# Kernel tuning notes

Measured on AMD Instinct MI355X. Metric: run time of the kernel, lower is better.

## Reference

```python
import jax, jax.numpy as jnp
import numpy as np
from jax import lax

L = 12  # db6 filter length
REC_LO = np.array([0.11154074335008017, 0.4946238903983854, 0.7511339080215775,
                   0.3152503517092432, -0.22626469396516913, -0.12976686756709563,
                   0.09750160558707936, 0.02752286553001629, -0.031582039318031156,
                   0.0005538422009938016, 0.004777257511010651, -0.00107730108499558])
DEC_LO = REC_LO[::-1]
_sgn = (-1.0) ** np.arange(L)
DEC_HI = -_sgn * REC_LO            # pywt dec_hi
REC_HI = _sgn * DEC_LO             # pywt rec_hi
# XLA conv = cross-correlation; pytorch_wavelets correlates with reversed dec filters
K_ANA = np.ascontiguousarray(np.stack([DEC_LO[::-1], DEC_HI[::-1]])[:, None, :])  # (2,1,12)
# conv_transpose(stride2, pad L-2) == dilate-by-2, pad 1, correlate with flipped rec filters
K_SYN = np.ascontiguousarray(np.stack([REC_LO[::-1], REC_HI[::-1]])[None, :, :])  # (1,2,12)
J = 8


def _afb(x):
    # one analysis level, symmetric mode (pytorch_wavelets afb1d)
    B, C, N = x.shape
    out = (N + L - 1) // 2
    p = 2 * (out - 1) - N + L
    xp = jnp.pad(x, ((0, 0), (0, 0), (p // 2, p - p // 2)), mode='symmetric')
    y = lax.conv_general_dilated(xp.reshape(B * C, 1, -1), jnp.asarray(K_ANA, x.dtype),
                                 (2,), 'VALID', dimension_numbers=('NCH', 'OIH', 'NCH'))
    y = y.reshape(B, C, 2, out)
    return y[:, :, 0], y[:, :, 1]


def _sfb(lo, hi):
    # one synthesis level (pytorch_wavelets sfb1d); crop lo to hi length first
    lo = lo[..., :hi.shape[-1]]
    B, C, N = lo.shape
    z = jnp.stack([lo, hi], 2).reshape(B * C, 2, N)
    y = lax.conv_general_dilated(z, jnp.asarray(K_SYN, lo.dtype), (1,), [(1, 1)],
                                 lhs_dilation=(2,), dimension_numbers=('NCH', 'OIH', 'NCH'))
    return y.reshape(B, C, -1)  # length 2N - L + 2


def _wave_conv(x, w1, w2):
    lo, highs = x, []
    for _ in range(J):
        lo, hi = _afb(lo)
        highs.append(hi)
    lo = jnp.einsum('bix,iox->box', lo, w1)
    highs[-1] = jnp.einsum('bix,iox->box', highs[-1], w2)
    for hi in highs[::-1]:
        lo = _sfb(lo, hi)
    return lo


def _branch(xg, fc0_w, fc0_b, ww1, ww2, cw, cb, fc1_w, fc1_b, fc2_w, fc2_b):
    v = jnp.transpose(xg @ fc0_w + fc0_b, (0, 2, 1))  # (B,C,S)
    for i in range(4):
        a = _wave_conv(v, ww1[i], ww2[i])
        b = jnp.einsum('bcs,oc->bos', v, cw[i]) + cb[i][None, :, None]
        v = a + b
        if i < 3:
            v = jax.nn.gelu(v, approximate=False)
    v = jnp.transpose(v, (0, 2, 1))
    v = jax.nn.gelu(v @ fc1_w + fc1_b, approximate=False)
    return v @ fc2_w + fc2_b


def setup_inputs() -> dict:
    key = jax.random.key(0)
    ks = iter(jax.random.split(key, 32))
    B, S, W, LV = 64, 1024, 64, 8
    d = {"x": jax.random.normal(next(ks), (B, S, 1), jnp.float32)}
    def params(pref):
        sc = 1.0 / (W * W)
        d[pref + "fc0_w"] = jax.random.normal(next(ks), (2, W), jnp.float32) * 0.5
        d[pref + "fc0_b"] = jax.random.normal(next(ks), (W,), jnp.float32) * 0.1
        d[pref + "wave_w1"] = sc * jax.random.uniform(next(ks), (4, W, W, LV + 6), jnp.float32)
        d[pref + "wave_w2"] = sc * jax.random.uniform(next(ks), (4, W, W, LV + 6), jnp.float32)
        d[pref + "cw"] = jax.random.normal(next(ks), (4, W, W), jnp.float32) * (1.0 / np.sqrt(W))
        d[pref + "cb"] = jax.random.normal(next(ks), (4, W), jnp.float32) * 0.05
        d[pref + "fc1_w"] = jax.random.normal(next(ks), (W, 128), jnp.float32) * (1.0 / np.sqrt(W))
        d[pref + "fc1_b"] = jax.random.normal(next(ks), (128,), jnp.float32) * 0.05
        d[pref + "fc2_w"] = jax.random.normal(next(ks), (128, 1), jnp.float32) * (1.0 / np.sqrt(128))
        d[pref + "fc2_b"] = jax.random.normal(next(ks), (1,), jnp.float32) * 0.05
    params("")
    params("nt_")
    return d


def reference(x, fc0_w, fc0_b, wave_w1, wave_w2, cw, cb, fc1_w, fc1_b, fc2_w, fc2_b,
              nt_fc0_w, nt_fc0_b, nt_wave_w1, nt_wave_w2, nt_cw, nt_cb,
              nt_fc1_w, nt_fc1_b, nt_fc2_w, nt_fc2_b):
    B, S, _ = x.shape
    grid = jnp.broadcast_to(jnp.linspace(0.0, 1.0, S, dtype=x.dtype)[None, :, None], (B, S, 1))
    xg = jnp.concatenate([x, grid], -1)
    y = _branch(xg, fc0_w, fc0_b, wave_w1, wave_w2, cw, cb, fc1_w, fc1_b, fc2_w, fc2_b)
    y_nt = _branch(xg, nt_fc0_w, nt_fc0_b, nt_wave_w1, nt_wave_w2, nt_cw, nt_cb,
                   nt_fc1_w, nt_fc1_b, nt_fc2_w, nt_fc2_b)
    return y + y_nt
```

## Files before the change

### kernel.cpp

```cpp
#include <hip/hip_runtime.h>
#include <hip/hip_bf16.h>
#include <math.h>


#define BDIM 64
#define SLEN 1024
#define WCH  64
#define BC   (BDIM*WCH)
#define NT   16

typedef short s16x8 __attribute__((ext_vector_type(8)));
typedef float f32x4 __attribute__((ext_vector_type(4)));
typedef unsigned short u16x4 __attribute__((ext_vector_type(4)));

constexpr float RLv[12] = {
    0.11154074335008017f, 0.4946238903983854f, 0.7511339080215775f,
    0.3152503517092432f, -0.22626469396516913f, -0.12976686756709563f,
    0.09750160558707936f, 0.02752286553001629f, -0.031582039318031156f,
    0.0005538422009938016f, 0.004777257511010651f, -0.00107730108499558f };
constexpr float AHv[12] = {
     RLv[11], -RLv[10],  RLv[9], -RLv[8],  RLv[7], -RLv[6],
     RLv[5],  -RLv[4],   RLv[3], -RLv[2],  RLv[1], -RLv[0] };
constexpr float SLv[12] = {
     RLv[11], RLv[10], RLv[9], RLv[8], RLv[7], RLv[6],
     RLv[5],  RLv[4],  RLv[3], RLv[2], RLv[1], RLv[0] };
constexpr float SHv[12] = {
    -RLv[0],  RLv[1], -RLv[2],  RLv[3], -RLv[4],  RLv[5],
    -RLv[6],  RLv[7], -RLv[8],  RLv[9], -RLv[10], RLv[11] };

__device__ __forceinline__ float gelu_f(float x) {
    float z = 0.7978845608f * (x + 0.044715f * x * x * x);
    return x / (1.0f + __expf(-2.0f * z));
}
__device__ __forceinline__ unsigned short f2bf(float f) {
    __hip_bfloat16 h = __float2bfloat16(f);
    union { __hip_bfloat16 h; unsigned short u; } cv; cv.h = h; return cv.u;
}
__device__ __forceinline__ float bf2f(unsigned short u) {
    union { unsigned short u; __hip_bfloat16 h; } cv; cv.u = u;
    return __bfloat162float(cv.h);
}
__device__ __forceinline__ void unpack_frag(const unsigned int* p8,
                                            s16x8* ah, s16x8* al) {
    uint4 a = *(const uint4*)p8;
    uint4 b = *(const uint4*)(p8 + 4);
    union { s16x8 v; unsigned int d[4]; } H, L;
    H.d[0] = __builtin_amdgcn_perm(a.y, a.x, 0x05040100u);
    H.d[1] = __builtin_amdgcn_perm(a.w, a.z, 0x05040100u);
    H.d[2] = __builtin_amdgcn_perm(b.y, b.x, 0x05040100u);
    H.d[3] = __builtin_amdgcn_perm(b.w, b.z, 0x05040100u);
    L.d[0] = __builtin_amdgcn_perm(a.y, a.x, 0x07060302u);
    L.d[1] = __builtin_amdgcn_perm(a.w, a.z, 0x07060302u);
    L.d[2] = __builtin_amdgcn_perm(b.y, b.x, 0x07060302u);
    L.d[3] = __builtin_amdgcn_perm(b.w, b.z, 0x07060302u);
    *ah = H.v; *al = L.v;
}

__device__ __forceinline__ int swz(int c, int s) {
    return c * 64 + ((((s >> 3) ^ (c & 7)) << 3) | (s & 7));
}
__device__ __forceinline__ int swz2(int s, int c) {
    return s * 64 + ((((c >> 3) ^ (s & 7)) << 3) | (c & 7));
}

__device__ __forceinline__ void proj2(
    const unsigned short* Phi, const unsigned short* Plo,
    const unsigned short* __restrict__ Ahi, const unsigned short* __restrict__ Alo,
    float* __restrict__ Ppart, int bb, int tile, int s0, int t)
{
    const int lane = t & 63;
    const int w    = t >> 6;
    const int qr   = lane >> 4;
    const int ln   = lane & 15;

    f32x4 pacc[2][2];
#pragma unroll
    for (int mt = 0; mt < 2; ++mt)
#pragma unroll
        for (int ni = 0; ni < 2; ++ni) pacc[mt][ni] = (f32x4){0.f,0.f,0.f,0.f};

#pragma unroll
    for (int kk = 0; kk < 2; ++kk) {
        const int bk = kk * 4 + qr;
        s16x8 pah[2], pal[2];
#pragma unroll
        for (int mt = 0; mt < 2; ++mt) {
            const int arow = (mt * 16 + ln) * SLEN + s0 + kk * 32 + qr * 8;
            pah[mt] = *(const s16x8*)&Ahi[arow];
            pal[mt] = *(const s16x8*)&Alo[arow];
        }
#pragma unroll
        for (int ni = 0; ni < 2; ++ni) {
            const int c = w * 32 + ni * 16 + ln;
            const int boff = c * 64 + ((bk ^ (c & 7)) << 3);
            s16x8 bh = *(const s16x8*)&Phi[boff];
            s16x8 bl = *(const s16x8*)&Plo[boff];
#pragma unroll
            for (int mt = 0; mt < 2; ++mt) {
                pacc[mt][ni] = __builtin_amdgcn_mfma_f32_16x16x32_bf16(pah[mt], bh, pacc[mt][ni], 0, 0, 0);
                pacc[mt][ni] = __builtin_amdgcn_mfma_f32_16x16x32_bf16(pal[mt], bh, pacc[mt][ni], 0, 0, 0);
                pacc[mt][ni] = __builtin_amdgcn_mfma_f32_16x16x32_bf16(pah[mt], bl, pacc[mt][ni], 0, 0, 0);
            }
        }
    }
#pragma unroll
    for (int mt = 0; mt < 2; ++mt)
#pragma unroll
        for (int ni = 0; ni < 2; ++ni) {
            const int c = w * 32 + ni * 16 + ln;
#pragma unroll
            for (int r = 0; r < 4; ++r) {
                const int xr = mt * 16 + qr * 4 + r;
                if (xr < 28)
                    Ppart[((size_t)(bb * NT + tile) * 28 + xr) * 64 + c] = pacc[mt][ni][r];
            }
        }
}

__global__ __launch_bounds__(256) void setup_kernel(
    const float* __restrict__ x,
    unsigned short* __restrict__ Ahi, unsigned short* __restrict__ Alo,
    unsigned short* __restrict__ MThi, unsigned short* __restrict__ MTlo,
    float* __restrict__ axbuf,
    const float* __restrict__ fc1w_0, const float* __restrict__ fc1w_1,
    const float* __restrict__ cw_0, const float* __restrict__ cw_1,
    unsigned short* __restrict__ w1hi, unsigned short* __restrict__ w1lo,
    unsigned short* __restrict__ cwPhi, unsigned short* __restrict__ cwPlo,
    unsigned short* __restrict__ Dhi,  unsigned short* __restrict__ Dlo)
{
    __shared__ float Af[1024];
    __shared__ float Bff[520];
    __shared__ float hib[14];
    const int t = threadIdx.x;

    if (blockIdx.x < 1024 || (blockIdx.x >= 1052 && blockIdx.x < 1118)) {
        const bool isA = (blockIdx.x < 1024);
        const int s0 = blockIdx.x;
        const int di = blockIdx.x - 1052;
        for (int i = t; i < SLEN; i += 256) {
            float v;
            if (isA)           v = (i == s0) ? 1.0f : 0.0f;
            else if (di < 64)  v = x[di * SLEN + i];
            else if (di == 64) v = (float)i * (1.0f / 1023.0f);
            else               v = 1.0f;
            Af[i] = v;
        }
        __syncthreads();

        const int NIN[8]  = {1024, 517, 264, 137, 74, 42, 26, 18};
        const int NOUT[8] = { 517, 264, 137,  74, 42, 26, 18, 14};
#pragma unroll
        for (int lev = 0; lev < 8; ++lev) {
            float* in  = (lev & 1) ? Bff : Af;
            float* out = (lev & 1) ? Af : Bff;
            const int nin = NIN[lev], nout = NOUT[lev];
            for (int m = t; m < nout; m += 256) {
                float alo = 0.f, ahi = 0.f;
#pragma unroll
                for (int tt = 0; tt < 12; ++tt) {
                    int jj = 2 * m + tt - 10;
                    if (jj < 0)         jj = -1 - jj;
                    else if (jj >= nin) jj = 2 * nin - 1 - jj;
                    float xv = in[jj];
                    alo += xv * RLv[tt];
                    if (lev == 7) ahi += xv * AHv[tt];
                }
                out[m] = alo;
                if (lev == 7) {
                    if (isA) {
                        unsigned short h1 = f2bf(alo);
                        Ahi[m * SLEN + s0] = h1;
                        Alo[m * SLEN + s0] = f2bf(alo - bf2f(h1));
                        unsigned short h2 = f2bf(ahi);
                        Ahi[(14 + m) * SLEN + s0] = h2;
                        Alo[(14 + m) * SLEN + s0] = f2bf(ahi - bf2f(h2));
                    } else {
                        axbuf[di * 28 + m]      = alo;
                        axbuf[di * 28 + 14 + m] = ahi;
                    }
                }
            }
            __syncthreads();
        }
        if (isA && t < 4) {
            Ahi[(28 + t) * SLEN + s0] = 0; Alo[(28 + t) * SLEN + s0] = 0;
            MThi[s0 * 32 + 28 + t] = 0;    MTlo[s0 * 32 + 28 + t] = 0;
        }
        return;
    }

    if (blockIdx.x >= 1118) {
        const int gid = (blockIdx.x - 1118) * 256 + t;
        for (int idx = gid; idx < 16384; idx += 2048) {
            int br = idx >> 13, r = idx & 8191;
            int h = r >> 6, c = r & 63;
            float f = (br ? fc1w_1 : fc1w_0)[c * 128 + h];
            unsigned short hh = f2bf(f);
            w1hi[idx] = hh;
            w1lo[idx] = f2bf(f - bf2f(hh));
        }
        for (int idx = gid; idx < 32768; idx += 2048) {
            int L = idx >> 13, br = (idx >> 12) & 1, e = idx & 4095;
            int k = e >> 6, o = e & 63;
            float val = (br ? cw_1 : cw_0)[(size_t)L * 4096 + o * 64 + k]
                      + ((k == o) ? 1.0f : 0.0f);
            unsigned short h = f2bf(val);
            const int off = (L * 2 + br) * 4096 + o * 64 + k;
            cwPhi[off] = h;
            cwPlo[off] = f2bf(val - bf2f(h));
        }
        for (int idx = gid; idx < 32768; idx += 2048) {
            int bb = idx >> 8, o = (idx >> 2) & 63, j = idx & 3;
            Dhi[bb * 2048 + o * 32 + 28 + j] = 0;
            Dlo[bb * 2048 + o * 32 + 28 + j] = 0;
        }
        return;
    }

    const int u = blockIdx.x - 1024;
    if (t < 14) {
        Af[t]  = (u < 14 && t == u) ? 1.0f : 0.0f;
        hib[t] = (u >= 14 && t == (u - 14)) ? 1.0f : 0.0f;
    }
    __syncthreads();

    const int NH[8] = {14, 18, 26, 42, 74, 137, 264, 517};
    const int NO[8] = {18, 26, 42, 74, 138, 264, 518, 1024};

#pragma unroll
    for (int s = 0; s < 8; ++s) {
        const float* lo = (s & 1) ? Bff : Af;
        float* out      = (s & 1) ? Af : Bff;
        const int N = NH[s], nout = NO[s];
        for (int m = t; m < nout; m += 256) {
            float acc = 0.f;
#pragma unroll
            for (int tt = 0; tt < 12; ++tt) {
                int uu = m + tt - 1;
                if ((uu & 1) == 0) {
                    int q = uu >> 1;
                    if (q < N) {
                        acc += lo[q] * SLv[tt];
                        if (s == 0) acc += hib[q] * SHv[tt];
                    }
                }
            }
            out[m] = acc;
        }
        __syncthreads();
    }
    for (int m = t; m < SLEN; m += 256) {
        float f = Af[m];
        unsigned short h = f2bf(f);
        MThi[m * 32 + u] = h;
        MTlo[m * 32 + u] = f2bf(f - bf2f(h));
    }
}

__global__ __launch_bounds__(256) void mix0_kernel(
    const float* __restrict__ axbuf,
    const float* __restrict__ fc0w_0, const float* __restrict__ fc0b_0,
    const float* __restrict__ fc0w_1, const float* __restrict__ fc0b_1,
    const float* __restrict__ w1_0, const float* __restrict__ w2_0,
    const float* __restrict__ w1_1, const float* __restrict__ w2_1,
    unsigned short* __restrict__ Dhi, unsigned short* __restrict__ Dlo)
{
    const int t = threadIdx.x;
    const int br  = blockIdx.x / 224;
    const int sub = blockIdx.x % 224;

    __shared__ float Ws[64][65];
    __shared__ float LO[8][64];
    const int o = t & 63;
    const int w = t >> 6;
    const int x  = sub >> 3;
    const int b0 = (sub & 7) << 3;

    const float* wbase = (x < 14) ? (br ? w1_1 : w1_0) : (br ? w2_1 : w2_0);
    const int xi = (x < 14) ? x : (x - 14);
    for (int idx = t; idx < 4096; idx += 256)
        Ws[idx >> 6][idx & 63] = wbase[(size_t)idx * 14 + xi];

    const float* fc0w = br ? fc0w_1 : fc0w_0;
    const float* fc0b = br ? fc0b_1 : fc0b_0;
    const float agv = axbuf[64 * 28 + x];
    const float a1v = axbuf[65 * 28 + x];
    const float w0o = fc0w[o];
    const float wgo = fc0w[WCH + o];
    const float b0o = fc0b[o];

#pragma unroll
    for (int j = 0; j < 2; ++j) {
        int bi = w + 4 * j;
        int b  = b0 + bi;
        float axv = axbuf[b * 28 + x];
        LO[bi][o] = axv * w0o + agv * wgo + a1v * b0o;
    }
    __syncthreads();

#pragma unroll
    for (int j = 0; j < 2; ++j) {
        int bi = w + 4 * j;
        int bb = br * 64 + b0 + bi;
        float acc = 0.f;
        for (int i = 0; i < 64; ++i)
            acc += LO[bi][i] * Ws[i][o];
        acc -= LO[bi][o];
        unsigned short h = f2bf(acc);
        Dhi[bb * 2048 + o * 32 + x] = h;
        Dlo[bb * 2048 + o * 32 + x] = f2bf(acc - bf2f(h));
    }
}

__global__ __launch_bounds__(256) void mix_kernel(
    const float* __restrict__ Ppart,
    const float* __restrict__ w1_0, const float* __restrict__ w2_0,
    const float* __restrict__ w1_1, const float* __restrict__ w2_1,
    unsigned short* __restrict__ Dhi, unsigned short* __restrict__ Dlo)
{
    const int t = threadIdx.x;
    const int br  = blockIdx.x / 224;
    const int sub = blockIdx.x % 224;

    __shared__ float Ws[64][65];
    __shared__ float LO[8][64];
    const int o = t & 63;
    const int w = t >> 6;
    const int x  = sub >> 3;
    const int b0 = (sub & 7) << 3;

    const float* wbase = (x < 14) ? (br ? w1_1 : w1_0) : (br ? w2_1 : w2_0);
    const int xi = (x < 14) ? x : (x - 14);
    for (int idx = t; idx < 4096; idx += 256)
        Ws[idx >> 6][idx & 63] = wbase[(size_t)idx * 14 + xi];

#pragma unroll
    for (int j = 0; j < 2; ++j) {
        int bi = w + 4 * j;
        int bb = br * 64 + b0 + bi;
        float s = 0.f;
        for (int tile = 0; tile < NT; ++tile)
            s += Ppart[((size_t)(bb * NT + tile) * 28 + x) * 64 + o];
        LO[bi][o] = s;
    }
    __syncthreads();

#pragma unroll
    for (int j = 0; j < 2; ++j) {
        int bi = w + 4 * j;
        int bb = br * 64 + b0 + bi;
        float acc = 0.f;
        for (int i = 0; i < 64; ++i)
            acc += LO[bi][i] * Ws[i][o];
        acc -= LO[bi][o];
        unsigned short h = f2bf(acc);
        Dhi[bb * 2048 + o * 32 + x] = h;
        Dlo[bb * 2048 + o * 32 + x] = f2bf(acc - bf2f(h));
    }
}

__global__ __launch_bounds__(128, 3) void layer_kernel(
    const unsigned int* __restrict__ vin0, const unsigned int* __restrict__ vin1,
    unsigned int* __restrict__ vout0, unsigned int* __restrict__ vout1,
    const unsigned short* __restrict__ MThi, const unsigned short* __restrict__ MTlo,
    const unsigned short* __restrict__ Ahi,  const unsigned short* __restrict__ Alo,
    const unsigned short* __restrict__ cwPhi, const unsigned short* __restrict__ cwPlo,
    const unsigned short* __restrict__ Dhi,   const unsigned short* __restrict__ Dlo,
    const float* __restrict__ cb_0, const float* __restrict__ cb_1,
    const float* __restrict__ fc0w_0, const float* __restrict__ fc0b_0,
    const float* __restrict__ fc0w_1, const float* __restrict__ fc0b_1,
    const float* __restrict__ xin,
    float* __restrict__ Ppart, int Lidx)
{
    __shared__ unsigned short Phi[4096];
    __shared__ unsigned short Plo[4096];

    const int t = threadIdx.x;
    const int bid = blockIdx.x;
    const int br  = bid >> 10;
    const int rem = bid & 1023;
    const int b    = rem >> 4;
    const int tile = rem & 15;
    const int s0   = tile << 6;
    const size_t bS = (size_t)b * SLEN;
    const unsigned int* vin = br ? vin1 : vin0;
    unsigned int* vout      = br ? vout1 : vout0;
    const float* cb = br ? cb_1 : cb_0;
    const float* f0w = br ? fc0w_1 : fc0w_0;
    const float* f0b = br ? fc0b_1 : fc0b_0;
    const int bb = br * 64 + b;
    const int cwbase = (Lidx * 2 + br) * 4096;

    const int lane = t & 63;
    const int w    = t >> 6;
    const int qr   = lane >> 4;
    const int ln   = lane & 15;

    s16x8 Bh[2][2], Bl[2][2];
#pragma unroll
    for (int kk = 0; kk < 2; ++kk)
#pragma unroll
        for (int ni = 0; ni < 2; ++ni) {
            const int o = w * 32 + ni * 16 + ln;
            const int boff = cwbase + o * 64 + kk * 32 + qr * 8;
            Bh[kk][ni] = *(const s16x8*)&cwPhi[boff];
            Bl[kk][ni] = *(const s16x8*)&cwPlo[boff];
        }
    s16x8 Dhf[2], Dlf[2];
#pragma unroll
    for (int ni = 0; ni < 2; ++ni) {
        const int o = w * 32 + ni * 16 + ln;
        const int boff = bb * 2048 + o * 32 + qr * 8;
        Dhf[ni] = *(const s16x8*)&Dhi[boff];
        Dlf[ni] = *(const s16x8*)&Dlo[boff];
    }
    float cbv[2];
#pragma unroll
    for (int ni = 0; ni < 2; ++ni) cbv[ni] = cb[w * 32 + ni * 16 + ln];

#pragma unroll
    for (int mi = 0; mi < 4; ++mi) {
        const int srow = mi * 16 + ln;
        f32x4 acc[2];
        acc[0] = (f32x4){0.f,0.f,0.f,0.f};
        acc[1] = (f32x4){0.f,0.f,0.f,0.f};

#pragma unroll
        for (int kk = 0; kk < 2; ++kk) {
            s16x8 ah, al;
            if (Lidx == 0) {
                const int s = s0 + srow;
                const float xv = xin[bS + s];
                const float gv = (float)s * (1.0f / 1023.0f);
#pragma unroll
                for (int j = 0; j < 8; ++j) {
                    const int c = kk * 32 + qr * 8 + j;
                    float val = xv * f0w[c] + gv * f0w[WCH + c] + f0b[c];
                    unsigned short h = f2bf(val);
                    ah[j] = (short)h;
                    al[j] = (short)f2bf(val - bf2f(h));
                }
            } else {
                const size_t aoff = (bS + s0 + srow) * 64 + kk * 32 + qr * 8;
                unpack_frag(&vin[aoff], &ah, &al);
            }
#pragma unroll
            for (int ni = 0; ni < 2; ++ni) {
                acc[ni] = __builtin_amdgcn_mfma_f32_16x16x32_bf16(ah, Bh[kk][ni], acc[ni], 0, 0, 0);
                acc[ni] = __builtin_amdgcn_mfma_f32_16x16x32_bf16(al, Bh[kk][ni], acc[ni], 0, 0, 0);
                acc[ni] = __builtin_amdgcn_mfma_f32_16x16x32_bf16(ah, Bl[kk][ni], acc[ni], 0, 0, 0);
            }
        }
        {
            const size_t aoff = (size_t)(s0 + srow) * 32 + qr * 8;
            s16x8 ah = *(const s16x8*)&MThi[aoff];
            s16x8 al = *(const s16x8*)&MTlo[aoff];
#pragma unroll
            for (int ni = 0; ni < 2; ++ni) {
                acc[ni] = __builtin_amdgcn_mfma_f32_16x16x32_bf16(ah, Dhf[ni], acc[ni], 0, 0, 0);
                acc[ni] = __builtin_amdgcn_mfma_f32_16x16x32_bf16(al, Dhf[ni], acc[ni], 0, 0, 0);
                acc[ni] = __builtin_amdgcn_mfma_f32_16x16x32_bf16(ah, Dlf[ni], acc[ni], 0, 0, 0);
            }
        }
#pragma unroll
        for (int ni = 0; ni < 2; ++ni) {
            const int o = w * 32 + ni * 16 + ln;
            u16x4 hv, lv;
#pragma unroll
            for (int r = 0; r < 4; ++r) {
                const int sl64 = mi * 16 + qr * 4 + r;
                float val = gelu_f(acc[ni][r] + cbv[ni]);
                unsigned short h = f2bf(val);
                unsigned short l = f2bf(val - bf2f(h));
                vout[(bS + s0 + sl64) * 64 + o] =
                    (unsigned int)h | ((unsigned int)l << 16);
                hv[r] = h;
                lv[r] = l;
            }
            const int a = swz(o, mi * 16 + qr * 4);
            *(u16x4*)&Phi[a] = hv;
            *(u16x4*)&Plo[a] = lv;
        }
    }

    proj2(Phi, Plo, Ahi, Alo, Ppart, bb, tile, s0, t);
}

__global__ __launch_bounds__(256, 2) void head_kernel(
    const unsigned int* __restrict__ vin0, const unsigned int* __restrict__ vin1,
    const unsigned short* __restrict__ MThi, const unsigned short* __restrict__ MTlo,
    const unsigned short* __restrict__ cwPhi, const unsigned short* __restrict__ cwPlo,
    const unsigned short* __restrict__ Dhi,   const unsigned short* __restrict__ Dlo,
    const float* __restrict__ cb_0, const float* __restrict__ cb_1,
    const unsigned short* __restrict__ w1hi, const unsigned short* __restrict__ w1lo,
    const float* __restrict__ fc1b_0, const float* __restrict__ fc2w_0,
    const float* __restrict__ fc2b_0,
    const float* __restrict__ fc1b_1, const float* __restrict__ fc2w_1,
    const float* __restrict__ fc2b_1,
    float* __restrict__ out)
{
    __shared__ unsigned short Vh[8192];
    __shared__ unsigned short Vl[8192];
    __shared__ float SP[4][64];

    const int t = threadIdx.x;
    const int bid = blockIdx.x;
    const int b    = bid >> 4;
    const int tile = bid & 15;
    const int s0   = tile << 6;
    const size_t bS = (size_t)b * SLEN;

    const int lane = t & 63;
    const int w    = t >> 6;
    const int br   = w >> 1;
    const int half = w & 1;
    const int qr   = lane >> 4;
    const int ln   = lane & 15;

    const unsigned int* vin = br ? vin1 : vin0;
    const float* cb   = (br ? cb_1 : cb_0) + 3 * WCH;
    const float* fc1b = br ? fc1b_1 : fc1b_0;
    const float* fc2w = br ? fc2w_1 : fc2w_0;
    const int bb = br * 64 + b;
    const int cwbase = (3 * 2 + br) * 4096;
    unsigned short* Vhp = Vh + br * 4096;
    unsigned short* Vlp = Vl + br * 4096;

    {
        s16x8 Bh[2][2], Bl[2][2];
#pragma unroll
        for (int kk = 0; kk < 2; ++kk)
#pragma unroll
            for (int ni = 0; ni < 2; ++ni) {
                const int o = half * 32 + ni * 16 + ln;
                const int boff = cwbase + o * 64 + kk * 32 + qr * 8;
                Bh[kk][ni] = *(const s16x8*)&cwPhi[boff];
                Bl[kk][ni] = *(const s16x8*)&cwPlo[boff];
            }
        s16x8 Dhf[2], Dlf[2];
#pragma unroll
        for (int ni = 0; ni < 2; ++ni) {
            const int o = half * 32 + ni * 16 + ln;
            const int boff = bb * 2048 + o * 32 + qr * 8;
            Dhf[ni] = *(const s16x8*)&Dhi[boff];
            Dlf[ni] = *(const s16x8*)&Dlo[boff];
        }
        float cbv[2];
#pragma unroll
        for (int ni = 0; ni < 2; ++ni) cbv[ni] = cb[half * 32 + ni * 16 + ln];

#pragma unroll
        for (int mi = 0; mi < 4; ++mi) {
            const int srow = mi * 16 + ln;
            f32x4 acc[2];
            acc[0] = (f32x4){0.f,0.f,0.f,0.f};
            acc[1] = (f32x4){0.f,0.f,0.f,0.f};

#pragma unroll
            for (int kk = 0; kk < 2; ++kk) {
                const size_t aoff = (bS + s0 + srow) * 64 + kk * 32 + qr * 8;
                s16x8 ah, al;
                unpack_frag(&vin[aoff], &ah, &al);
#pragma unroll
                for (int ni = 0; ni < 2; ++ni) {
                    acc[ni] = __builtin_amdgcn_mfma_f32_16x16x32_bf16(ah, Bh[kk][ni], acc[ni], 0, 0, 0);
                    acc[ni] = __builtin_amdgcn_mfma_f32_16x16x32_bf16(al, Bh[kk][ni], acc[ni], 0, 0, 0);
                    acc[ni] = __builtin_amdgcn_mfma_f32_16x16x32_bf16(ah, Bl[kk][ni], acc[ni], 0, 0, 0);
                }
            }
            {
                const size_t aoff = (size_t)(s0 + srow) * 32 + qr * 8;
                s16x8 ah = *(const s16x8*)&MThi[aoff];
                s16x8 al = *(const s16x8*)&MTlo[aoff];
#pragma unroll
                for (int ni = 0; ni < 2; ++ni) {
                    acc[ni] = __builtin_amdgcn_mfma_f32_16x16x32_bf16(ah, Dhf[ni], acc[ni], 0, 0, 0);
                    acc[ni] = __builtin_amdgcn_mfma_f32_16x16x32_bf16(al, Dhf[ni], acc[ni], 0, 0, 0);
                    acc[ni] = __builtin_amdgcn_mfma_f32_16x16x32_bf16(ah, Dlf[ni], acc[ni], 0, 0, 0);
                }
            }
#pragma unroll
            for (int ni = 0; ni < 2; ++ni) {
                const int o = half * 32 + ni * 16 + ln;
#pragma unroll
                for (int r = 0; r < 4; ++r) {
                    const int sl64 = mi * 16 + qr * 4 + r;
                    float val = acc[ni][r] + cbv[ni];
                    unsigned short h = f2bf(val);
                    unsigned short l = f2bf(val - bf2f(h));
                    const int a = swz2(sl64, o);
                    Vhp[a] = h;
                    Vlp[a] = l;
                }
            }
        }
    }
    __syncthreads();

    s16x8 Wh[2][4], Wl[2][4];
#pragma unroll
    for (int kk = 0; kk < 2; ++kk)
#pragma unroll
        for (int ni = 0; ni < 4; ++ni) {
            const int h = half * 64 + ni * 16 + ln;
            const int boff = br * 8192 + h * 64 + kk * 32 + qr * 8;
            Wh[kk][ni] = *(const s16x8*)&w1hi[boff];
            Wl[kk][ni] = *(const s16x8*)&w1lo[boff];
        }
    float b1v[4], w2v[4];
#pragma unroll
    for (int ni = 0; ni < 4; ++ni) {
        b1v[ni] = fc1b[half * 64 + ni * 16 + ln];
        w2v[ni] = fc2w[half * 64 + ni * 16 + ln];
    }

#pragma unroll
    for (int mi = 0; mi < 4; ++mi) {
        f32x4 acc1[4];
#pragma unroll
        for (int ni = 0; ni < 4; ++ni) acc1[ni] = (f32x4){0.f,0.f,0.f,0.f};

#pragma unroll
        for (int kk = 0; kk < 2; ++kk) {
            const int blk = kk * 4 + qr;
            const int sl  = mi * 16 + ln;
            const int a   = sl * 64 + ((blk ^ (sl & 7)) << 3);
            s16x8 ah = *(const s16x8*)&Vhp[a];
            s16x8 al = *(const s16x8*)&Vlp[a];
#pragma unroll
            for (int ni = 0; ni < 4; ++ni) {
                acc1[ni] = __builtin_amdgcn_mfma_f32_16x16x32_bf16(ah, Wh[kk][ni], acc1[ni], 0, 0, 0);
                acc1[ni] = __builtin_amdgcn_mfma_f32_16x16x32_bf16(al, Wh[kk][ni], acc1[ni], 0, 0, 0);
                acc1[ni] = __builtin_amdgcn_mfma_f32_16x16x32_bf16(ah, Wl[kk][ni], acc1[ni], 0, 0, 0);
            }
        }
        float partial[4] = {0.f, 0.f, 0.f, 0.f};
#pragma unroll
        for (int ni = 0; ni < 4; ++ni) {
#pragma unroll
            for (int r = 0; r < 4; ++r)
                partial[r] += gelu_f(acc1[ni][r] + b1v[ni]) * w2v[ni];
        }
#pragma unroll
        for (int r = 0; r < 4; ++r) {
            partial[r] += __shfl_xor(partial[r], 1, 64);
            partial[r] += __shfl_xor(partial[r], 2, 64);
            partial[r] += __shfl_xor(partial[r], 4, 64);
            partial[r] += __shfl_xor(partial[r], 8, 64);
        }
        if (ln == 0) {
#pragma unroll
            for (int r = 0; r < 4; ++r)
                SP[w][mi * 16 + qr * 4 + r] = partial[r];
        }
    }
    __syncthreads();

    if (t < 64) {
        const float bias = fc2b_0[0] + fc2b_1[0];
        out[bS + s0 + t] = SP[0][t] + SP[1][t] + SP[2][t] + SP[3][t] + bias;
    }
}

extern "C" void kernel_launch(void* const* d_in, const int* in_sizes, int n_in,
                              void* d_out, int out_size, void* d_ws, size_t ws_size,
                              hipStream_t stream)
{
    const float* x = (const float*)d_in[0];
    const float* P[2][10];
    for (int br = 0; br < 2; ++br)
        for (int k = 0; k < 10; ++k)
            P[br][k] = (const float*)d_in[1 + br * 10 + k];

    char* p = (char*)d_ws;
    const size_t PL = (size_t)BC * SLEN * 4;
    unsigned int* vplane[4];
    for (int i = 0; i < 4; ++i) { vplane[i] = (unsigned int*)p; p += PL; }
    unsigned short* Ahi  = (unsigned short*)p; p += 32 * SLEN * 2;
    unsigned short* Alo  = (unsigned short*)p; p += 32 * SLEN * 2;
    unsigned short* MThi = (unsigned short*)p; p += SLEN * 32 * 2;
    unsigned short* MTlo = (unsigned short*)p; p += SLEN * 32 * 2;
    float* Ppart = (float*)p;                  p += (size_t)128 * NT * 28 * 64 * 4;
    unsigned short* cwPhi = (unsigned short*)p; p += 8 * 4096 * 2;
    unsigned short* cwPlo = (unsigned short*)p; p += 8 * 4096 * 2;
    unsigned short* Dhi   = (unsigned short*)p; p += (size_t)128 * 2048 * 2;
    unsigned short* Dlo   = (unsigned short*)p; p += (size_t)128 * 2048 * 2;
    unsigned short* w1hi  = (unsigned short*)p; p += 2 * 8192 * 2;
    unsigned short* w1lo  = (unsigned short*)p; p += 2 * 8192 * 2;
    float* axbuf          = (float*)p;          p += 66 * 28 * 4;

    unsigned int *v0a = vplane[0], *v0b = vplane[1];
    unsigned int *v1a = vplane[2], *v1b = vplane[3];

    setup_kernel<<<1126, 256, 0, stream>>>(
        x, Ahi, Alo, MThi, MTlo, axbuf,
        P[0][6], P[1][6], P[0][4], P[1][4],
        w1hi, w1lo, cwPhi, cwPlo, Dhi, Dlo);

    mix0_kernel<<<448, 256, 0, stream>>>(
        axbuf, P[0][0], P[0][1], P[1][0], P[1][1],
        P[0][2], P[0][3], P[1][2], P[1][3],
        Dhi, Dlo);

    for (int i = 0; i < 3; ++i) {
        layer_kernel<<<2048, 128, 0, stream>>>(
            v0a, v1a, v0b, v1b,
            MThi, MTlo, Ahi, Alo, cwPhi, cwPlo, Dhi, Dlo,
            P[0][5] + (size_t)i * WCH, P[1][5] + (size_t)i * WCH,
            P[0][0], P[0][1], P[1][0], P[1][1], x,
            Ppart, i);
        unsigned int* tmp;
        tmp = v0a; v0a = v0b; v0b = tmp;
        tmp = v1a; v1a = v1b; v1b = tmp;

        mix_kernel<<<448, 256, 0, stream>>>(
            Ppart,
            P[0][2] + (size_t)(i + 1) * WCH * WCH * 14, P[0][3] + (size_t)(i + 1) * WCH * WCH * 14,
            P[1][2] + (size_t)(i + 1) * WCH * WCH * 14, P[1][3] + (size_t)(i + 1) * WCH * WCH * 14,
            Dhi, Dlo);
    }

    head_kernel<<<1024, 256, 0, stream>>>(
        v0a, v1a,
        MThi, MTlo, cwPhi, cwPlo, Dhi, Dlo,
        P[0][5] + (size_t)3 * WCH, P[1][5] + (size_t)3 * WCH,
        w1hi, w1lo,
        P[0][7], P[0][8], P[0][9],
        P[1][7], P[1][8], P[1][9],
        (float*)d_out);
}
```

Before: 252.1 us.

## Pre-transpose mixing weights, split MFMA accumulators, and prefetch activation fragments

Adds setup blocks that transpose the per-mode mixing weights (w1/w2) into a contiguous [x][k][o] layout. The mix kernels can then load them with coalesced reads instead of stride-14 gathers. The three-term bf16 split MFMA chains are split into two independent accumulators, which shortens the dependent MFMA chain. The next row-tile's activation fragments are register-prefetched in the layer and head loops to hide global load latency. The costs are an extra workspace buffer, 16 more setup blocks, and higher register pressure.

```diff
diff --git a/kernel.cpp b/kernel.cpp
--- a/kernel.cpp
+++ b/kernel.cpp
@@ -40,10 +40,8 @@
     union { unsigned short u; __hip_bfloat16 h; } cv; cv.u = u;
     return __bfloat162float(cv.h);
 }
-__device__ __forceinline__ void unpack_frag(const unsigned int* p8,
-                                            s16x8* ah, s16x8* al) {
-    uint4 a = *(const uint4*)p8;
-    uint4 b = *(const uint4*)(p8 + 4);
+__device__ __forceinline__ void unpack_frag2(uint4 a, uint4 b,
+                                             s16x8* ah, s16x8* al) {
     union { s16x8 v; unsigned int d[4]; } H, L;
     H.d[0] = __builtin_amdgcn_perm(a.y, a.x, 0x05040100u);
     H.d[1] = __builtin_amdgcn_perm(a.w, a.z, 0x05040100u);
@@ -73,22 +71,28 @@
     const int qr   = lane >> 4;
     const int ln   = lane & 15;
 
-    f32x4 pacc[2][2];
+    s16x8 pah[2][2], pal[2][2];
+#pragma unroll
+    for (int kk = 0; kk < 2; ++kk)
+#pragma unroll
+        for (int mt = 0; mt < 2; ++mt) {
+            const int arow = (mt * 16 + ln) * SLEN + s0 + kk * 32 + qr * 8;
+            pah[kk][mt] = *(const s16x8*)&Ahi[arow];
+            pal[kk][mt] = *(const s16x8*)&Alo[arow];
+        }
+
+    f32x4 pP[2][2], pS[2][2];
 #pragma unroll
     for (int mt = 0; mt < 2; ++mt)
 #pragma unroll
-        for (int ni = 0; ni < 2; ++ni) pacc[mt][ni] = (f32x4){0.f,0.f,0.f,0.f};
+        for (int ni = 0; ni < 2; ++ni) {
+            pP[mt][ni] = (f32x4){0.f,0.f,0.f,0.f};
+            pS[mt][ni] = (f32x4){0.f,0.f,0.f,0.f};
+        }
 
 #pragma unroll
     for (int kk = 0; kk < 2; ++kk) {
         const int bk = kk * 4 + qr;
-        s16x8 pah[2], pal[2];
-#pragma unroll
-        for (int mt = 0; mt < 2; ++mt) {
-            const int arow = (mt * 16 + ln) * SLEN + s0 + kk * 32 + qr * 8;
-            pah[mt] = *(const s16x8*)&Ahi[arow];
-            pal[mt] = *(const s16x8*)&Alo[arow];
-        }
 #pragma unroll
         for (int ni = 0; ni < 2; ++ni) {
             const int c = w * 32 + ni * 16 + ln;
@@ -97,9 +101,9 @@
             s16x8 bl = *(const s16x8*)&Plo[boff];
 #pragma unroll
             for (int mt = 0; mt < 2; ++mt) {
-                pacc[mt][ni] = __builtin_amdgcn_mfma_f32_16x16x32_bf16(pah[mt], bh, pacc[mt][ni], 0, 0, 0);
-                pacc[mt][ni] = __builtin_amdgcn_mfma_f32_16x16x32_bf16(pal[mt], bh, pacc[mt][ni], 0, 0, 0);
-                pacc[mt][ni] = __builtin_amdgcn_mfma_f32_16x16x32_bf16(pah[mt], bl, pacc[mt][ni], 0, 0, 0);
+                pP[mt][ni] = __builtin_amdgcn_mfma_f32_16x16x32_bf16(pah[kk][mt], bh, pP[mt][ni], 0, 0, 0);
+                pS[mt][ni] = __builtin_amdgcn_mfma_f32_16x16x32_bf16(pal[kk][mt], bh, pS[mt][ni], 0, 0, 0);
+                pS[mt][ni] = __builtin_amdgcn_mfma_f32_16x16x32_bf16(pah[kk][mt], bl, pS[mt][ni], 0, 0, 0);
             }
         }
     }
@@ -108,11 +112,12 @@
 #pragma unroll
         for (int ni = 0; ni < 2; ++ni) {
             const int c = w * 32 + ni * 16 + ln;
+            f32x4 pv = pP[mt][ni] + pS[mt][ni];
 #pragma unroll
             for (int r = 0; r < 4; ++r) {
                 const int xr = mt * 16 + qr * 4 + r;
                 if (xr < 28)
-                    Ppart[((size_t)(bb * NT + tile) * 28 + xr) * 64 + c] = pacc[mt][ni][r];
+                    Ppart[((size_t)(bb * NT + tile) * 28 + xr) * 64 + c] = pv[r];
             }
         }
 }
@@ -124,9 +129,12 @@
     float* __restrict__ axbuf,
     const float* __restrict__ fc1w_0, const float* __restrict__ fc1w_1,
     const float* __restrict__ cw_0, const float* __restrict__ cw_1,
+    const float* __restrict__ w1_0, const float* __restrict__ w2_0,
+    const float* __restrict__ w1_1, const float* __restrict__ w2_1,
     unsigned short* __restrict__ w1hi, unsigned short* __restrict__ w1lo,
     unsigned short* __restrict__ cwPhi, unsigned short* __restrict__ cwPlo,
-    unsigned short* __restrict__ Dhi,  unsigned short* __restrict__ Dlo)
+    unsigned short* __restrict__ Dhi,  unsigned short* __restrict__ Dlo,
+    float* __restrict__ WsT)
 {
     __shared__ float Af[1024];
     __shared__ float Bff[520];
@@ -189,6 +197,24 @@
         return;
     }
 
+    if (blockIdx.x >= 1126) {
+        const int wsb = blockIdx.x - 1126;
+        const int L = wsb >> 2, br = (wsb >> 1) & 1, which = wsb & 1;
+        const float* src = (which ? (br ? w2_1 : w2_0) : (br ? w1_1 : w1_0))
+                         + (size_t)L * 64 * 64 * 14;
+        const size_t dbase = ((size_t)(L * 2 + br) * 28 + which * 14) * 4096;
+        for (int e = t; e < 4096; e += 256) {
+            const float* sp = src + (size_t)e * 14;
+            float v[14];
+#pragma unroll
+            for (int xi = 0; xi < 14; ++xi) v[xi] = sp[xi];
+#pragma unroll
+            for (int xi = 0; xi < 14; ++xi)
+                WsT[dbase + (size_t)xi * 4096 + e] = v[xi];
+        }
+        return;
+    }
+
     if (blockIdx.x >= 1118) {
         const int gid = (blockIdx.x - 1118) * 256 + t;
         for (int idx = gid; idx < 16384; idx += 2048) {
@@ -261,8 +287,7 @@
     const float* __restrict__ axbuf,
     const float* __restrict__ fc0w_0, const float* __restrict__ fc0b_0,
     const float* __restrict__ fc0w_1, const float* __restrict__ fc0b_1,
-    const float* __restrict__ w1_0, const float* __restrict__ w2_0,
-    const float* __restrict__ w1_1, const float* __restrict__ w2_1,
+    const float* __restrict__ WsT0,
     unsigned short* __restrict__ Dhi, unsigned short* __restrict__ Dlo)
 {
     const int t = threadIdx.x;
@@ -276,10 +301,9 @@
     const int x  = sub >> 3;
     const int b0 = (sub & 7) << 3;
 
-    const float* wbase = (x < 14) ? (br ? w1_1 : w1_0) : (br ? w2_1 : w2_0);
-    const int xi = (x < 14) ? x : (x - 14);
+    const float* wsrc = WsT0 + ((size_t)(br * 28 + x)) * 4096;
     for (int idx = t; idx < 4096; idx += 256)
-        Ws[idx >> 6][idx & 63] = wbase[(size_t)idx * 14 + xi];
+        Ws[idx >> 6][idx & 63] = wsrc[idx];
 
     const float* fc0w = br ? fc0w_1 : fc0w_0;
     const float* fc0b = br ? fc0b_1 : fc0b_0;
@@ -314,8 +338,7 @@
 
 __global__ __launch_bounds__(256) void mix_kernel(
     const float* __restrict__ Ppart,
-    const float* __restrict__ w1_0, const float* __restrict__ w2_0,
-    const float* __restrict__ w1_1, const float* __restrict__ w2_1,
+    const float* __restrict__ WsTL,
     unsigned short* __restrict__ Dhi, unsigned short* __restrict__ Dlo)
 {
     const int t = threadIdx.x;
@@ -329,10 +352,9 @@
     const int x  = sub >> 3;
     const int b0 = (sub & 7) << 3;
 
-    const float* wbase = (x < 14) ? (br ? w1_1 : w1_0) : (br ? w2_1 : w2_0);
-    const int xi = (x < 14) ? x : (x - 14);
+    const float* wsrc = WsTL + ((size_t)(br * 28 + x)) * 4096;
     for (int idx = t; idx < 4096; idx += 256)
-        Ws[idx >> 6][idx & 63] = wbase[(size_t)idx * 14 + xi];
+        Ws[idx >> 6][idx & 63] = wsrc[idx];
 
 #pragma unroll
     for (int j = 0; j < 2; ++j) {
@@ -418,58 +440,86 @@
 #pragma unroll
     for (int ni = 0; ni < 2; ++ni) cbv[ni] = cb[w * 32 + ni * 16 + ln];
 
+    uint4 vb[2][2];
+    float xpf = 0.f;
+    if (Lidx == 0) {
+        xpf = xin[bS + s0 + ln];
+    } else {
+        const size_t a0 = (bS + s0 + ln) * 64 + qr * 8;
+        vb[0][0] = *(const uint4*)&vin[a0];
+        vb[0][1] = *(const uint4*)&vin[a0 + 4];
+        vb[1][0] = *(const uint4*)&vin[a0 + 32];
+        vb[1][1] = *(const uint4*)&vin[a0 + 36];
+    }
+
 #pragma unroll
     for (int mi = 0; mi < 4; ++mi) {
         const int srow = mi * 16 + ln;
-        f32x4 acc[2];
-        acc[0] = (f32x4){0.f,0.f,0.f,0.f};
-        acc[1] = (f32x4){0.f,0.f,0.f,0.f};
+        uint4 vn[2][2];
+        float xnf = 0.f;
+        if (mi < 3) {
+            if (Lidx == 0) {
+                xnf = xin[bS + s0 + (mi + 1) * 16 + ln];
+            } else {
+                const size_t an = (bS + s0 + (mi + 1) * 16 + ln) * 64 + qr * 8;
+                vn[0][0] = *(const uint4*)&vin[an];
+                vn[0][1] = *(const uint4*)&vin[an + 4];
+                vn[1][0] = *(const uint4*)&vin[an + 32];
+                vn[1][1] = *(const uint4*)&vin[an + 36];
+            }
+        }
+
+        f32x4 accP[2], accS[2];
+#pragma unroll
+        for (int ni = 0; ni < 2; ++ni) {
+            accP[ni] = (f32x4){0.f,0.f,0.f,0.f};
+            accS[ni] = (f32x4){0.f,0.f,0.f,0.f};
+        }
 
 #pragma unroll
         for (int kk = 0; kk < 2; ++kk) {
             s16x8 ah, al;
             if (Lidx == 0) {
                 const int s = s0 + srow;
-                const float xv = xin[bS + s];
                 const float gv = (float)s * (1.0f / 1023.0f);
 #pragma unroll
                 for (int j = 0; j < 8; ++j) {
                     const int c = kk * 32 + qr * 8 + j;
-                    float val = xv * f0w[c] + gv * f0w[WCH + c] + f0b[c];
+                    float val = xpf * f0w[c] + gv * f0w[WCH + c] + f0b[c];
                     unsigned short h = f2bf(val);
                     ah[j] = (short)h;
                     al[j] = (short)f2bf(val - bf2f(h));
                 }
             } else {
-                const size_t aoff = (bS + s0 + srow) * 64 + kk * 32 + qr * 8;
-                unpack_frag(&vin[aoff], &ah, &al);
+                unpack_frag2(vb[kk][0], vb[kk][1], &ah, &al);
             }
 #pragma unroll
             for (int ni = 0; ni < 2; ++ni) {
-                acc[ni] = __builtin_amdgcn_mfma_f32_16x16x32_bf16(ah, Bh[kk][ni], acc[ni], 0, 0, 0);
-                acc[ni] = __builtin_amdgcn_mfma_f32_16x16x32_bf16(al, Bh[kk][ni], acc[ni], 0, 0, 0);
-                acc[ni] = __builtin_amdgcn_mfma_f32_16x16x32_bf16(ah, Bl[kk][ni], acc[ni], 0, 0, 0);
+                accP[ni] = __builtin_amdgcn_mfma_f32_16x16x32_bf16(ah, Bh[kk][ni], accP[ni], 0, 0, 0);
+                accS[ni] = __builtin_amdgcn_mfma_f32_16x16x32_bf16(al, Bh[kk][ni], accS[ni], 0, 0, 0);
+                accS[ni] = __builtin_amdgcn_mfma_f32_16x16x32_bf16(ah, Bl[kk][ni], accS[ni], 0, 0, 0);
             }
         }
         {
             const size_t aoff = (size_t)(s0 + srow) * 32 + qr * 8;
-            s16x8 ah = *(const s16x8*)&MThi[aoff];
-            s16x8 al = *(const s16x8*)&MTlo[aoff];
+            s16x8 mh = *(const s16x8*)&MThi[aoff];
+            s16x8 ml = *(const s16x8*)&MTlo[aoff];
 #pragma unroll
             for (int ni = 0; ni < 2; ++ni) {
-                acc[ni] = __builtin_amdgcn_mfma_f32_16x16x32_bf16(ah, Dhf[ni], acc[ni], 0, 0, 0);
-                acc[ni] = __builtin_amdgcn_mfma_f32_16x16x32_bf16(al, Dhf[ni], acc[ni], 0, 0, 0);
-                acc[ni] = __builtin_amdgcn_mfma_f32_16x16x32_bf16(ah, Dlf[ni], acc[ni], 0, 0, 0);
+                accP[ni] = __builtin_amdgcn_mfma_f32_16x16x32_bf16(mh, Dhf[ni], accP[ni], 0, 0, 0);
+                accS[ni] = __builtin_amdgcn_mfma_f32_16x16x32_bf16(ml, Dhf[ni], accS[ni], 0, 0, 0);
+                accS[ni] = __builtin_amdgcn_mfma_f32_16x16x32_bf16(mh, Dlf[ni], accS[ni], 0, 0, 0);
             }
         }
 #pragma unroll
         for (int ni = 0; ni < 2; ++ni) {
             const int o = w * 32 + ni * 16 + ln;
+            f32x4 acc = accP[ni] + accS[ni];
             u16x4 hv, lv;
 #pragma unroll
             for (int r = 0; r < 4; ++r) {
                 const int sl64 = mi * 16 + qr * 4 + r;
-                float val = gelu_f(acc[ni][r] + cbv[ni]);
+                float val = gelu_f(acc[r] + cbv[ni]);
                 unsigned short h = f2bf(val);
                 unsigned short l = f2bf(val - bf2f(h));
                 vout[(bS + s0 + sl64) * 64 + o] =
@@ -480,6 +530,14 @@
             const int a = swz(o, mi * 16 + qr * 4);
             *(u16x4*)&Phi[a] = hv;
             *(u16x4*)&Plo[a] = lv;
+        }
+        if (mi < 3) {
+            if (Lidx == 0) {
+                xpf = xnf;
+            } else {
+                vb[0][0] = vn[0][0]; vb[0][1] = vn[0][1];
+                vb[1][0] = vn[1][0]; vb[1][1] = vn[1][1];
+            }
         }
     }
 
@@ -549,43 +607,63 @@
 #pragma unroll
         for (int ni = 0; ni < 2; ++ni) cbv[ni] = cb[half * 32 + ni * 16 + ln];
 
+        uint4 vb[2][2];
+        {
+            const size_t a0 = (bS + s0 + ln) * 64 + qr * 8;
+            vb[0][0] = *(const uint4*)&vin[a0];
+            vb[0][1] = *(const uint4*)&vin[a0 + 4];
+            vb[1][0] = *(const uint4*)&vin[a0 + 32];
+            vb[1][1] = *(const uint4*)&vin[a0 + 36];
+        }
+
 #pragma unroll
         for (int mi = 0; mi < 4; ++mi) {
+            uint4 vn[2][2];
+            if (mi < 3) {
+                const size_t an = (bS + s0 + (mi + 1) * 16 + ln) * 64 + qr * 8;
+                vn[0][0] = *(const uint4*)&vin[an];
+                vn[0][1] = *(const uint4*)&vin[an + 4];
+                vn[1][0] = *(const uint4*)&vin[an + 32];
+                vn[1][1] = *(const uint4*)&vin[an + 36];
+            }
             const int srow = mi * 16 + ln;
-            f32x4 acc[2];
-            acc[0] = (f32x4){0.f,0.f,0.f,0.f};
-            acc[1] = (f32x4){0.f,0.f,0.f,0.f};
+            f32x4 accP[2], accS[2];
+#pragma unroll
+            for (int ni = 0; ni < 2; ++ni) {
+                accP[ni] = (f32x4){0.f,0.f,0.f,0.f};
+                accS[ni] = (f32x4){0.f,0.f,0.f,0.f};
+            }
 
 #pragma unroll
             for (int kk = 0; kk < 2; ++kk) {
-                const size_t aoff = (bS + s0 + srow) * 64 + kk * 32 + qr * 8;
                 s16x8 ah, al;
-                unpack_frag(&vin[aoff], &ah, &al);
+                unpack_frag2(vb[kk][0], vb[kk][1], &ah, &al);
 #pragma unroll
                 for (int ni = 0; ni < 2; ++ni) {
-                    acc[ni] = __builtin_amdgcn_mfma_f32_16x16x32_bf16(ah, Bh[kk][ni], acc[ni], 0, 0, 0);
-                    acc[ni] = __builtin_amdgcn_mfma_f32_16x16x32_bf16(al, Bh[kk][ni], acc[ni], 0, 0, 0);
-                    acc[ni] = __builtin_amdgcn_mfma_f32_16x16x32_bf16(ah, Bl[kk][ni], acc[ni], 0, 0, 0);
+                    accP[ni] = __builtin_amdgcn_mfma_f32_16x16x32_bf16(ah, Bh[kk][ni], accP[ni], 0, 0, 0);
+                    accS[ni] = __builtin_amdgcn_mfma_f32_16x16x32_bf16(al, Bh[kk][ni], accS[ni], 0, 0, 0);
+                    accS[ni] = __builtin_amdgcn_mfma_f32_16x16x32_bf16(ah, Bl[kk][ni], accS[ni], 0, 0, 0);
                 }
             }
             {
                 const size_t aoff = (size_t)(s0 + srow) * 32 + qr * 8;
-                s16x8 ah = *(const s16x8*)&MThi[aoff];
-                s16x8 al = *(const s16x8*)&MTlo[aoff];
+                s16x8 mh = *(const s16x8*)&MThi[aoff];
+                s16x8 ml = *(const s16x8*)&MTlo[aoff];
 #pragma unroll
                 for (int ni = 0; ni < 2; ++ni) {
-                    acc[ni] = __builtin_amdgcn_mfma_f32_16x16x32_bf16(ah, Dhf[ni], acc[ni], 0, 0, 0);
-                    acc[ni] = __builtin_amdgcn_mfma_f32_16x16x32_bf16(al, Dhf[ni], acc[ni], 0, 0, 0);
-                    acc[ni] = __builtin_amdgcn_mfma_f32_16x16x32_bf16(ah, Dlf[ni], acc[ni], 0, 0, 0);
+                    accP[ni] = __builtin_amdgcn_mfma_f32_16x16x32_bf16(mh, Dhf[ni], accP[ni], 0, 0, 0);
+                    accS[ni] = __builtin_amdgcn_mfma_f32_16x16x32_bf16(ml, Dhf[ni], accS[ni], 0, 0, 0);
+                    accS[ni] = __builtin_amdgcn_mfma_f32_16x16x32_bf16(mh, Dlf[ni], accS[ni], 0, 0, 0);
                 }
             }
 #pragma unroll
             for (int ni = 0; ni < 2; ++ni) {
                 const int o = half * 32 + ni * 16 + ln;
+                f32x4 acc = accP[ni] + accS[ni];
 #pragma unroll
                 for (int r = 0; r < 4; ++r) {
                     const int sl64 = mi * 16 + qr * 4 + r;
-                    float val = acc[ni][r] + cbv[ni];
+                    float val = acc[r] + cbv[ni];
                     unsigned short h = f2bf(val);
                     unsigned short l = f2bf(val - bf2f(h));
                     const int a = swz2(sl64, o);
@@ -593,6 +671,10 @@
                     Vlp[a] = l;
                 }
             }
+            if (mi < 3) {
+                vb[0][0] = vn[0][0]; vb[0][1] = vn[0][1];
+                vb[1][0] = vn[1][0]; vb[1][1] = vn[1][1];
+            }
         }
     }
     __syncthreads();
@@ -616,9 +698,12 @@
 
 #pragma unroll
     for (int mi = 0; mi < 4; ++mi) {
-        f32x4 acc1[4];
-#pragma unroll
-        for (int ni = 0; ni < 4; ++ni) acc1[ni] = (f32x4){0.f,0.f,0.f,0.f};
+        f32x4 a1P[4], a1S[4];
+#pragma unroll
+        for (int ni = 0; ni < 4; ++ni) {
+            a1P[ni] = (f32x4){0.f,0.f,0.f,0.f};
+            a1S[ni] = (f32x4){0.f,0.f,0.f,0.f};
+        }
 
 #pragma unroll
         for (int kk = 0; kk < 2; ++kk) {
@@ -629,17 +714,18 @@
             s16x8 al = *(const s16x8*)&Vlp[a];
 #pragma unroll
             for (int ni = 0; ni < 4; ++ni) {
-                acc1[ni] = __builtin_amdgcn_mfma_f32_16x16x32_bf16(ah, Wh[kk][ni], acc1[ni], 0, 0, 0);
-                acc1[ni] = __builtin_amdgcn_mfma_f32_16x16x32_bf16(al, Wh[kk][ni], acc1[ni], 0, 0, 0);
-                acc1[ni] = __builtin_amdgcn_mfma_f32_16x16x32_bf16(ah, Wl[kk][ni], acc1[ni], 0, 0, 0);
+                a1P[ni] = __builtin_amdgcn_mfma_f32_16x16x32_bf16(ah, Wh[kk][ni], a1P[ni], 0, 0, 0);
+                a1S[ni] = __builtin_amdgcn_mfma_f32_16x16x32_bf16(al, Wh[kk][ni], a1S[ni], 0, 0, 0);
+                a1S[ni] = __builtin_amdgcn_mfma_f32_16x16x32_bf16(ah, Wl[kk][ni], a1S[ni], 0, 0, 0);
             }
         }
         float partial[4] = {0.f, 0.f, 0.f, 0.f};
 #pragma unroll
         for (int ni = 0; ni < 4; ++ni) {
+            f32x4 acc1 = a1P[ni] + a1S[ni];
 #pragma unroll
             for (int r = 0; r < 4; ++r)
-                partial[r] += gelu_f(acc1[ni][r] + b1v[ni]) * w2v[ni];
+                partial[r] += gelu_f(acc1[r] + b1v[ni]) * w2v[ni];
         }
 #pragma unroll
         for (int r = 0; r < 4; ++r) {
@@ -688,19 +774,20 @@
     unsigned short* w1hi  = (unsigned short*)p; p += 2 * 8192 * 2;
     unsigned short* w1lo  = (unsigned short*)p; p += 2 * 8192 * 2;
     float* axbuf          = (float*)p;          p += 66 * 28 * 4;
+    float* WsT            = (float*)p;          p += (size_t)4 * 2 * 28 * 4096 * 4;
 
     unsigned int *v0a = vplane[0], *v0b = vplane[1];
     unsigned int *v1a = vplane[2], *v1b = vplane[3];
 
-    setup_kernel<<<1126, 256, 0, stream>>>(
+    setup_kernel<<<1142, 256, 0, stream>>>(
         x, Ahi, Alo, MThi, MTlo, axbuf,
         P[0][6], P[1][6], P[0][4], P[1][4],
-        w1hi, w1lo, cwPhi, cwPlo, Dhi, Dlo);
+        P[0][2], P[0][3], P[1][2], P[1][3],
+        w1hi, w1lo, cwPhi, cwPlo, Dhi, Dlo, WsT);
 
     mix0_kernel<<<448, 256, 0, stream>>>(
         axbuf, P[0][0], P[0][1], P[1][0], P[1][1],
-        P[0][2], P[0][3], P[1][2], P[1][3],
-        Dhi, Dlo);
+        WsT, Dhi, Dlo);
 
     for (int i = 0; i < 3; ++i) {
         layer_kernel<<<2048, 128, 0, stream>>>(
@@ -715,8 +802,7 @@
 
         mix_kernel<<<448, 256, 0, stream>>>(
             Ppart,
-            P[0][2] + (size_t)(i + 1) * WCH * WCH * 14, P[0][3] + (size_t)(i + 1) * WCH * WCH * 14,
-            P[1][2] + (size_t)(i + 1) * WCH * WCH * 14, P[1][3] + (size_t)(i + 1) * WCH * WCH * 14,
+            WsT + (size_t)(i + 1) * 2 * 28 * 4096,
             Dhi, Dlo);
     }
 
```

New measurement: 252.8 us. Within noise of the previous version (+0.3%).
